# Kernel tuning notes

Hardware: AMD Instinct MI355X
Metric: run time of the kernel (lower is better)

## Reference

```python
import jax, jax.numpy as jnp
import numpy as np
import math

B, S = 4, 1024
V, D, L, H, F, MAXLEN = 32000, 1024, 6, 16, 4096, 2048
DH = D // H
NUM_BUCKETS, MAX_DIST = 32, 256
REL_SCALE = 64.0 ** 0.5
EPS = 1e-5


def setup_inputs() -> dict:
    key = jax.random.key(0)
    ks = iter(jax.random.split(key, 32))
    sd = 0.02
    inp = {
        'src': jax.random.randint(next(ks), (B, S), 0, V),
        'src_mask': jnp.ones((B, 1, 1, S), dtype=jnp.int32),
        'tok_emb': jax.random.normal(next(ks), (V, D), jnp.float32) * sd,
        'pos_emb': jax.random.normal(next(ks), (MAXLEN, D), jnp.float32) * sd,
        'Wq': jax.random.normal(next(ks), (L, D, D), jnp.float32) * sd,
        'bq': jnp.zeros((L, D), jnp.float32),
        'Wk': jax.random.normal(next(ks), (L, D, D), jnp.float32) * sd,
        'bk': jnp.zeros((L, D), jnp.float32),
        'Wv': jax.random.normal(next(ks), (L, D, D), jnp.float32) * sd,
        'bv': jnp.zeros((L, D), jnp.float32),
        'Wo': jax.random.normal(next(ks), (L, D, D), jnp.float32) * sd,
        'bo': jnp.zeros((L, D), jnp.float32),
        'rel_bias': jax.random.normal(next(ks), (L, NUM_BUCKETS, H), jnp.float32) * sd,
        'ln1_g': jnp.ones((L, D), jnp.float32),
        'ln1_b': jnp.zeros((L, D), jnp.float32),
        'W1': jax.random.normal(next(ks), (L, D, F), jnp.float32) * sd,
        'b1': jnp.zeros((L, F), jnp.float32),
        'W2': jax.random.normal(next(ks), (L, F, D), jnp.float32) * sd,
        'b2': jnp.zeros((L, D), jnp.float32),
        'ln2_g': jnp.ones((L, D), jnp.float32),
        'ln2_b': jnp.zeros((L, D), jnp.float32),
    }
    return inp


def _rel_pos_bucket(seq_len):
    # non-causal bucketing (T5-style), matching the torch source
    q = jnp.arange(seq_len)
    k = jnp.arange(seq_len)
    n = q[:, None] - k[None, :]          # == -(k - q)
    nb = NUM_BUCKETS // 2                # 16
    ret = (n < 0).astype(jnp.int32) * nb
    n = jnp.abs(n)
    max_exact = nb // 2                  # 8
    is_small = n < max_exact
    val_large = max_exact + (
        jnp.log(jnp.maximum(n, 1).astype(jnp.float32) / max_exact)
        / math.log(MAX_DIST / max_exact) * (nb - max_exact)
    ).astype(jnp.int32)
    val_large = jnp.minimum(val_large, nb - 1)
    return ret + jnp.where(is_small, n, val_large)  # [S,S] in [0,32)


def _layer_norm(x, g, b):
    mu = jnp.mean(x, axis=-1, keepdims=True)
    var = jnp.var(x, axis=-1, keepdims=True)
    return (x - mu) * jax.lax.rsqrt(var + EPS) * g + b


def reference(src, src_mask, tok_emb, pos_emb, Wq, bq, Wk, bk, Wv, bv, Wo, bo,
              rel_bias, ln1_g, ln1_b, W1, b1, W2, b2, ln2_g, ln2_b):
    seq_len = src.shape[1]
    bucket = _rel_pos_bucket(seq_len)                      # [S,S] int
    x = tok_emb[src] * jnp.sqrt(jnp.float32(D)) + pos_emb[jnp.arange(seq_len)][None]
    scale = jnp.sqrt(jnp.float32(DH))
    neg = jnp.float32(-1e10)

    def layer(x, p):
        (wq, bq_, wk, bk_, wv, bv_, wo, bo_, rb, g1, b1_, w1, bb1, w2, bb2, g2, b2_) = p
        Q = (x @ wq + bq_).reshape(B, seq_len, H, DH)
        K = (x @ wk + bk_).reshape(B, seq_len, H, DH)
        Vv = (x @ wv + bv_).reshape(B, seq_len, H, DH)
        energy = jnp.einsum('bqhd,bkhd->bhqk', Q, K) / scale
        energy = jnp.where(src_mask == 0, neg, energy)
        bias = rb[bucket]                                  # [S,S,H]
        energy = energy + jnp.transpose(bias, (2, 0, 1))[None] * REL_SCALE
        attn = jax.nn.softmax(energy, axis=-1)
        o = jnp.einsum('bhqk,bkhd->bqhd', attn, Vv).reshape(B, seq_len, D)
        o = o @ wo + bo_
        x = _layer_norm(x + o, g1, b1_)
        f = jax.nn.relu(x @ w1 + bb1) @ w2 + bb2
        x = _layer_norm(x + f, g2, b2_)
        return x, None

    params = (Wq, bq, Wk, bk, Wv, bv, Wo, bo, rel_bias,
              ln1_g, ln1_b, W1, b1, W2, b2, ln2_g, ln2_b)
    x, _ = jax.lax.scan(layer, x, params)
    return x
```

## Files before the change

### kernel.cpp

```cpp
#include <hip/hip_runtime.h>

#define B_ 4
#define S_ 1024
#define D_ 1024
#define F_ 4096
#define H_ 16
#define L_ 6
#define M_ (B_*S_)

#define LOG2E 1.44269504088896f

typedef unsigned short u16;
typedef __attribute__((ext_vector_type(4))) unsigned short u16x4;
typedef __attribute__((ext_vector_type(8))) short s16x8;
typedef __attribute__((ext_vector_type(8))) __bf16 bf16x8;
typedef __attribute__((ext_vector_type(4))) float f32x4;

typedef const __attribute__((address_space(1))) unsigned int gu32;
typedef __attribute__((address_space(3))) unsigned int su32;

__device__ __forceinline__ u16 f2bf(float f) {
  union { float f; unsigned u; } v; v.f = f;
  unsigned u = v.u;
  return (u16)((u + 0x7fffu + ((u >> 16) & 1u)) >> 16);
}
__device__ __forceinline__ float bf2f(u16 h) {
  union { unsigned u; float f; } v; v.u = (unsigned)h << 16; return v.f;
}

__device__ __forceinline__ f32x4 mfma16(s16x8 a, s16x8 b, f32x4 c) {
  return __builtin_amdgcn_mfma_f32_16x16x32_bf16(
      __builtin_bit_cast(bf16x8, a), __builtin_bit_cast(bf16x8, b), c, 0, 0, 0);
}

__device__ __forceinline__ void gload16(const void* g, void* s) {
  __builtin_amdgcn_global_load_lds((gu32*)g, (su32*)s, 16, 0, 0);
}

template<int OUTMODE>
__device__ __forceinline__ void gemm128_body(
    const u16* __restrict__ A, const u16* __restrict__ Bt,
    const float* __restrict__ b0, const float* __restrict__ b1,
    const float* __restrict__ b2, u16* __restrict__ Ch,
    u16* __restrict__ Vt, int N, int K, int kbeg, int kend)
{
  __shared__ __align__(16) u16 As[128 * 64];
  __shared__ __align__(16) u16 Bs[128 * 64];
  const int tid = threadIdx.x, lane = tid & 63, w = tid >> 6;
  const int bm = blockIdx.x * 128, bn = blockIdx.y * 128;
  const int wm = (w >> 1) * 64, wn = (w & 1) * 64;

  f32x4 acc[4][4];
#pragma unroll
  for (int i = 0; i < 4; i++)
#pragma unroll
    for (int j = 0; j < 4; j++) acc[i][j] = {0.f, 0.f, 0.f, 0.f};

  for (int k0 = kbeg; k0 < kend; k0 += 64) {
    __syncthreads();
#pragma unroll
    for (int i = 0; i < 4; i++) {
      const int flat = i * 4096 + w * 1024 + lane * 16;
      const int row = flat >> 7, ce = (flat & 127) >> 1;
      gload16(A + (size_t)(bm + row) * K + k0 + ce, As + i * 2048 + w * 512);
      gload16(Bt + (size_t)(bn + row) * K + k0 + ce, Bs + i * 2048 + w * 512);
    }
    __syncthreads();
#pragma unroll
    for (int kk = 0; kk < 2; kk++) {
      s16x8 af[4], bf[4];
#pragma unroll
      for (int mf = 0; mf < 4; mf++)
        af[mf] = *(const s16x8*)&As[(wm + mf * 16 + (lane & 15)) * 64 + kk * 32 + (lane >> 4) * 8];
#pragma unroll
      for (int nf = 0; nf < 4; nf++)
        bf[nf] = *(const s16x8*)&Bs[(wn + nf * 16 + (lane & 15)) * 64 + kk * 32 + (lane >> 4) * 8];
#pragma unroll
      for (int mf = 0; mf < 4; mf++)
#pragma unroll
        for (int nf = 0; nf < 4; nf++)
          acc[mf][nf] = mfma16(af[mf], bf[nf], acc[mf][nf]);
    }
  }

  if (OUTMODE == 3) {
    const int zz = bn >> 10;
    const int lcb = (bn & 1023) + wn;
    const float* bp = (zz == 0) ? b0 : (zz == 1) ? b1 : b2;
    if (zz == 2) {
      const int b = bm >> 10;
#pragma unroll
      for (int nf = 0; nf < 4; nf++) {
        const int dh2 = lcb + nf * 16 + (lane & 15);
        const int hq = dh2 >> 6, dh = dh2 & 63;
        const float bv = bp[dh2];
        u16* vrow = Vt + ((size_t)((b << 4) + hq) * 64 + dh) * S_;
#pragma unroll
        for (int mf = 0; mf < 4; mf++) {
          const int s0 = (bm & 1023) + wm + mf * 16 + ((lane >> 4) << 2);
          u16x4 hv;
#pragma unroll
          for (int j = 0; j < 4; j++) hv[j] = f2bf(acc[mf][nf][j] + bv);
          *(u16x4*)(vrow + s0) = hv;
        }
      }
    } else {
      const float sc = (zz == 0) ? (0.125f * LOG2E) : 1.0f;
      u16* Outz = Ch + (size_t)zz * M_ * D_;
#pragma unroll
      for (int nf = 0; nf < 4; nf++) {
        const int col = lcb + nf * 16 + (lane & 15);
        const float bv = bp[col];
#pragma unroll
        for (int mf = 0; mf < 4; mf++) {
#pragma unroll
          for (int j = 0; j < 4; j++) {
            const int row = bm + wm + mf * 16 + ((lane >> 4) << 2) + j;
            Outz[(size_t)row * D_ + col] = f2bf((acc[mf][nf][j] + bv) * sc);
          }
        }
      }
    }
  } else {
#pragma unroll
    for (int nf = 0; nf < 4; nf++) {
      const int col = bn + wn + nf * 16 + (lane & 15);
#pragma unroll
      for (int mf = 0; mf < 4; mf++) {
#pragma unroll
        for (int j = 0; j < 4; j++) {
          const int row = bm + wm + mf * 16 + ((lane >> 4) << 2) + j;
          Ch[(size_t)row * N + col] = f2bf(acc[mf][nf][j]);
        }
      }
    }
  }
}

__global__ __launch_bounds__(256, 3) void gemm_qkvf(
    const u16* __restrict__ A, const u16* __restrict__ WT,
    const float* __restrict__ bq, const float* __restrict__ bk,
    const float* __restrict__ bv, u16* __restrict__ Out, u16* __restrict__ Vt)
{
  gemm128_body<3>(A, WT, bq, bk, bv, Out, Vt, 3 * D_, D_, 0, D_);
}

__global__ __launch_bounds__(256, 3) void gemm_osplit2(
    const u16* __restrict__ A, const u16* __restrict__ WT,
    u16* __restrict__ P)
{
  const int z = blockIdx.z;
  gemm128_body<1>(A, WT, nullptr, nullptr, nullptr,
                  P + (size_t)z * M_ * D_, nullptr, D_, D_, z * 512, z * 512 + 512);
}

__device__ __forceinline__ s16x8 readfrag(const u16* half, int r, int kk, int hi4) {
  const int c = (kk * 64 + hi4 * 16) ^ ((r & 7) << 4);
  return *(const s16x8*)((const char*)half + r * 128 + c);
}

__device__ __forceinline__ void stage_half(
    const u16* __restrict__ src, int ldk, u16* lds_half, int w, int lane)
{
#pragma unroll
  for (int j = 0; j < 2; j++) {
    const int flat = j * 8192 + w * 1024 + lane * 16;
    const int row = flat >> 7;
    const int kb = (flat & 127) ^ ((row & 7) << 4);
    gload16(src + (size_t)row * ldk + (kb >> 1), lds_half + j * 4096 + w * 512);
  }
}

#define BAR     asm volatile("s_barrier" ::: "memory")
#define PH_PRE  asm volatile("s_barrier" ::: "memory"); __builtin_amdgcn_s_setprio(1)
#define PH_POST __builtin_amdgcn_s_setprio(0); __builtin_amdgcn_sched_barrier(0)
#define VM4     asm volatile("s_waitcnt vmcnt(4)" ::: "memory")
#define VM0     asm volatile("s_waitcnt vmcnt(0)" ::: "memory")

#define READ_B(bufhalf) do { \
  _Pragma("unroll") for (int nf = 0; nf < 4; nf++) \
  _Pragma("unroll") for (int kk = 0; kk < 2; kk++) \
    bfr[nf][kk] = readfrag(bufhalf, rb0 + nf * 16 + lo16, kk, hi4); } while (0)
#define READ_A(bufhalf, Q) do { \
  _Pragma("unroll") for (int m = 0; m < 2; m++) \
  _Pragma("unroll") for (int kk = 0; kk < 2; kk++) \
    af[m][kk] = readfrag(bufhalf, (2 * (Q) + m) * 16 + lo16, kk, hi4); } while (0)
#define DO_MFMA(Q) do { \
  _Pragma("unroll") for (int kk = 0; kk < 2; kk++) \
  _Pragma("unroll") for (int m = 0; m < 2; m++) \
  _Pragma("unroll") for (int nf = 0; nf < 4; nf++) \
    acc[2 * (Q) + m][nf] = mfma16(af[m][kk], bfr[nf][kk], acc[2 * (Q) + m][nf]); } while (0)

template<int OUTMODE>
__device__ __forceinline__ void gemm256_body(
    const u16* __restrict__ A, const u16* __restrict__ Bt,
    const float* __restrict__ bias, u16* __restrict__ Ch,
    int N, int K, int kbeg, int kslice)
{
  __shared__ __align__(16) u16 As[2][2][8192];
  __shared__ __align__(16) u16 Bs[2][2][8192];
  const int tid = threadIdx.x, lane = tid & 63, w = tid >> 6;
  const int wr = w >> 2, wc = w & 3;
  const int lo16 = lane & 15, hi4 = lane >> 4;
  const int bm = blockIdx.x * 256, bn = blockIdx.y * 256;
  const int rb0 = (wc & 1) * 64;

  const u16* Abase = A + (size_t)bm * K + kbeg;
  const u16* Bbase = Bt + (size_t)bn * K + kbeg;
  const size_t h1 = (size_t)128 * K;
  const int NT = kslice >> 6, NI = NT >> 1;

  f32x4 acc[8][4];
#pragma unroll
  for (int i = 0; i < 8; i++)
#pragma unroll
    for (int j = 0; j < 4; j++) acc[i][j] = {0.f, 0.f, 0.f, 0.f};

  stage_half(Abase,           K, As[0][0], w, lane);
  stage_half(Abase + h1,      K, As[0][1], w, lane);
  stage_half(Bbase,           K, Bs[0][0], w, lane);
  stage_half(Bbase + h1,      K, Bs[0][1], w, lane);
  stage_half(Abase + 64,      K, As[1][0], w, lane);
  stage_half(Abase + h1 + 64, K, As[1][1], w, lane);
  stage_half(Bbase + 64,      K, Bs[1][0], w, lane);
  stage_half(Bbase + h1 + 64, K, Bs[1][1], w, lane);
  asm volatile("s_waitcnt vmcnt(8)" ::: "memory");
  BAR;

  const u16* Ae = As[0][wr]; const u16* Ao = As[1][wr];
  const u16* Be = Bs[0][wc >> 1]; const u16* Bo = Bs[1][wc >> 1];
  s16x8 af[2][2], bfr[4][2];

  for (int it = 0; it < NI - 1; ++it) {
    READ_B(Be); READ_A(Ae, 0);
    if (it > 0) {
      stage_half(Abase +      (size_t)(2 * it + 1) * 64, K, As[1][0], w, lane);
      stage_half(Abase + h1 + (size_t)(2 * it + 1) * 64, K, As[1][1], w, lane);
    }
    PH_PRE; DO_MFMA(0); PH_POST; BAR;
    READ_A(Ae, 1);
    stage_half(Bbase +      (size_t)(2 * it + 2) * 64, K, Bs[0][0], w, lane);
    PH_PRE; DO_MFMA(1); PH_POST; BAR;
    READ_A(Ae, 2);
    stage_half(Bbase + h1 + (size_t)(2 * it + 2) * 64, K, Bs[0][1], w, lane);
    PH_PRE; DO_MFMA(2); PH_POST; BAR;
    READ_A(Ae, 3);
    PH_PRE; DO_MFMA(3); PH_POST; VM4; BAR;
    READ_B(Bo); READ_A(Ao, 0);
    stage_half(Abase +      (size_t)(2 * it + 2) * 64, K, As[0][0], w, lane);
    stage_half(Abase + h1 + (size_t)(2 * it + 2) * 64, K, As[0][1], w, lane);
    PH_PRE; DO_MFMA(0); PH_POST; BAR;
    READ_A(Ao, 1);
    stage_half(Bbase +      (size_t)(2 * it + 3) * 64, K, Bs[1][0], w, lane);
    PH_PRE; DO_MFMA(1); PH_POST; BAR;
    READ_A(Ao, 2);
    stage_half(Bbase + h1 + (size_t)(2 * it + 3) * 64, K, Bs[1][1], w, lane);
    PH_PRE; DO_MFMA(2); PH_POST; BAR;
    READ_A(Ao, 3);
    PH_PRE; DO_MFMA(3); PH_POST; VM4; BAR;
  }
  READ_B(Be); READ_A(Ae, 0);
  stage_half(Abase +      (size_t)(NT - 1) * 64, K, As[1][0], w, lane);
  stage_half(Abase + h1 + (size_t)(NT - 1) * 64, K, As[1][1], w, lane);
  PH_PRE; DO_MFMA(0); PH_POST; BAR;
  READ_A(Ae, 1);             PH_PRE; DO_MFMA(1); PH_POST; BAR;
  READ_A(Ae, 2);             PH_PRE; DO_MFMA(2); PH_POST; BAR;
  READ_A(Ae, 3);             PH_PRE; DO_MFMA(3); PH_POST; VM0; BAR;
  READ_B(Bo); READ_A(Ao, 0); PH_PRE; DO_MFMA(0); PH_POST; BAR;
  READ_A(Ao, 1);             PH_PRE; DO_MFMA(1); PH_POST; BAR;
  READ_A(Ao, 2);             PH_PRE; DO_MFMA(2); PH_POST; BAR;
  READ_A(Ao, 3);             PH_PRE; DO_MFMA(3); PH_POST;

  const int row0 = bm + wr * 128, col0 = bn + wc * 64;
#pragma unroll
  for (int nf = 0; nf < 4; nf++) {
    const int col = col0 + nf * 16 + lo16;
    const float bv = (OUTMODE == 2) ? bias[col] : 0.f;
#pragma unroll
    for (int mf = 0; mf < 8; mf++) {
#pragma unroll
      for (int j = 0; j < 4; j++) {
        const int row = row0 + mf * 16 + hi4 * 4 + j;
        float v = acc[mf][nf][j];
        if (OUTMODE == 2) v = fmaxf(v + bv, 0.f);
        Ch[(size_t)row * N + col] = f2bf(v);
      }
    }
  }
}

__global__ __launch_bounds__(512, 2) void gemm_ffn1(
    const u16* __restrict__ A, const u16* __restrict__ WT,
    const float* __restrict__ bias, u16* __restrict__ Out)
{
  gemm256_body<2>(A, WT, bias, Out, F_, D_, 0, D_);
}

__global__ __launch_bounds__(512, 2) void gemm_ffn2sp4(
    const u16* __restrict__ A, const u16* __restrict__ WT,
    u16* __restrict__ P)
{
  const int z = blockIdx.z;
  gemm256_body<4>(A, WT, nullptr, P + (size_t)z * M_ * D_,
                  D_, F_, z * 1024, 1024);
}

__global__ __launch_bounds__(256) void transpose_layer(
    const float* __restrict__ Wq, const float* __restrict__ Wk,
    const float* __restrict__ Wv, const float* __restrict__ Wo,
    const float* __restrict__ W1, const float* __restrict__ W2,
    u16* __restrict__ WT)
{
  __shared__ float tl[64][65];
  int bt = blockIdx.x;
  const float* src; u16* dst; int Rsrc, Csrc, cx, cy;
  if (bt < 1024) {
    const int m = bt >> 8; const int t = bt & 255;
    src = (m == 0) ? Wq : (m == 1) ? Wk : (m == 2) ? Wv : Wo;
    dst = WT + (size_t)m * 1024 * 1024;
    Rsrc = 1024; Csrc = 1024; cx = t & 15; cy = t >> 4;
  } else if (bt < 2048) {
    const int t = bt - 1024;
    src = W1; dst = WT + (size_t)4 * 1024 * 1024;
    Rsrc = 1024; Csrc = 4096; cx = t & 63; cy = t >> 6;
  } else {
    const int t = bt - 2048;
    src = W2; dst = WT + (size_t)8 * 1024 * 1024;
    Rsrc = 4096; Csrc = 1024; cx = t & 15; cy = t >> 4;
  }
  const int r0 = cy * 64, c0 = cx * 64;
  const int tid = threadIdx.x;
  const int rl = tid >> 2, q = tid & 3;
  const float* sp = src + (size_t)(r0 + rl) * Csrc + c0 + q * 16;
#pragma unroll
  for (int i = 0; i < 4; i++) {
    const float4 v = *(const float4*)(sp + i * 4);
    tl[rl][q * 16 + i * 4 + 0] = v.x;
    tl[rl][q * 16 + i * 4 + 1] = v.y;
    tl[rl][q * 16 + i * 4 + 2] = v.z;
    tl[rl][q * 16 + i * 4 + 3] = v.w;
  }
  __syncthreads();
#pragma unroll
  for (int it = 0; it < 2; it++) {
    const int idx = tid + it * 256;
    const int cl = idx >> 3, seg = idx & 7;
    const int rw0 = seg * 8;
    s16x8 v8;
#pragma unroll
    for (int u = 0; u < 8; u++) v8[u] = (short)f2bf(tl[rw0 + u][cl]);
    *(s16x8*)(dst + (size_t)(c0 + cl) * Rsrc + r0 + rw0) = v8;
  }
}

__global__ __launch_bounds__(256) void build_lut(
    const float* __restrict__ rb, float* __restrict__ lut_g)
{
  const int h = blockIdx.x, l = blockIdx.y;
  for (int idx = threadIdx.x; idx < 2048; idx += 256) {
    const int rel = idx - 1024;
    const int ret = rel < 0 ? 16 : 0;
    const int n = rel < 0 ? -rel : rel;
    int bu;
    if (n < 8) bu = ret + n;
    else {
      const float t = logf((float)n * 0.125f) * (8.0f / 3.4657359027997265f);
      int vl = 8 + (int)t;
      if (vl > 15) vl = 15;
      bu = ret + vl;
    }
    lut_g[(size_t)(l * H_ + h) * 2048 + idx] = rb[l * 512 + bu * 16 + h] * (8.0f * LOG2E);
  }
}

__global__ __launch_bounds__(256) void mask2neg(
    const int* __restrict__ mask, u16* __restrict__ mf)
{
  const int i = blockIdx.x * 256 + threadIdx.x;
  if (i < B_ * S_) mf[i] = mask[i] ? (u16)0 : f2bf(-1e10f * LOG2E);
}

__device__ __forceinline__ s16x8 lds_swz(const u16* base, int row, int cb) {
  const int addr = row * 128 + (cb ^ ((row & 7) << 4));
  return *(const s16x8*)((const char*)base + addr);
}

#define ATTN_STAGE(t, buf) do { \
  const int kt2 = (t) * 64; \
  const int flat2 = tid * 16; \
  const int row2 = flat2 >> 7; \
  const int ce2 = ((flat2 & 127) ^ ((row2 & 7) << 4)) >> 1; \
  gload16(Kb + (size_t)(bS + kt2 + row2) * D_ + hh + ce2, Ks[buf] + w * 512); \
  gload16(Vt + (size_t)(bh * 64 + row2) * S_ + kt2 + ce2, Vs[buf] + w * 512); \
} while (0)

__global__ __launch_bounds__(512, 2) void attn_kernel(
    const u16* __restrict__ Qb, const u16* __restrict__ Kb,
    const u16* __restrict__ Vt, const u16* __restrict__ mask16,
    const float* __restrict__ lut_g, u16* __restrict__ AO)
{
  __shared__ __align__(16) float lut[2048];
  __shared__ __align__(16) u16 maskf[1024];
  __shared__ __align__(16) u16 Ks[2][64 * 64];
  __shared__ __align__(16) u16 Vs[2][64 * 64];
  __shared__ __align__(16) u16 Ps[8][16 * 68];

  const int tid = threadIdx.x;
  const int lane = tid & 63;
  const int w = tid >> 6;
  const int bh = blockIdx.x;
  const int b = bh >> 4, h = bh & 15;
  const int q0 = blockIdx.y * 128 + w * 16;
  const int bS = b * S_, hh = h * 64;
  const int lo16 = lane & 15, hi4 = lane >> 4;

  const float* lsrc = lut_g + (size_t)h * 2048;
  gload16(lsrc + w * 256 + lane * 4, lut + w * 256);
  if (w < 2)
    gload16(mask16 + bS + w * 512 + lane * 8, maskf + w * 512);

  s16x8 qf[2];
#pragma unroll
  for (int kk = 0; kk < 2; kk++)
    qf[kk] = *(const s16x8*)(Qb + (size_t)(bS + q0 + lo16) * D_ + hh +
                             kk * 32 + hi4 * 8);

  s16x8 onesf;
#pragma unroll
  for (int u = 0; u < 8; u++) onesf[u] = (short)((lo16 == 0) ? 0x3F80 : 0);

  f32x4 oacc[5];
#pragma unroll
  for (int i = 0; i < 5; i++) oacc[i] = {0.f, 0.f, 0.f, 0.f};

  ATTN_STAGE(0, 0);
  asm volatile("s_waitcnt vmcnt(0) lgkmcnt(0)" ::: "memory");
  __builtin_amdgcn_s_barrier();

  for (int t = 0; t < S_ / 64; ++t) {
    const int cur = t & 1;
    const int kt = t * 64;
    if (t < S_ / 64 - 1) ATTN_STAGE(t + 1, cur ^ 1);

    f32x4 sacc[4];
#pragma unroll
    for (int i = 0; i < 4; i++) sacc[i] = {0.f, 0.f, 0.f, 0.f};
#pragma unroll
    for (int kk = 0; kk < 2; kk++) {
      const int cb = kk * 64 + hi4 * 16;
#pragma unroll
      for (int nf = 0; nf < 4; nf++) {
        const s16x8 kb = lds_swz(Ks[cur], nf * 16 + lo16, cb);
        sacc[nf] = mfma16(qf[kk], kb, sacc[nf]);
      }
    }

    float kmf[4];
#pragma unroll
    for (int nf = 0; nf < 4; nf++)
      kmf[nf] = bf2f(maskf[kt + nf * 16 + lo16]);

    const int lidx0 = q0 + hi4 * 4 + 1024 - kt - lo16;
#pragma unroll
    for (int j = 0; j < 4; j++) {
      const int lrow = (hi4 << 2) + j;
#pragma unroll
      for (int nf = 0; nf < 4; nf++) {
        const float s = sacc[nf][j] + kmf[nf] + lut[lidx0 + j - nf * 16];
        Ps[w][lrow * 68 + nf * 16 + lo16] = f2bf(__builtin_amdgcn_exp2f(s));
      }
    }

#pragma unroll
    for (int kk = 0; kk < 2; kk++) {
      const s16x8 pa = *(const s16x8*)&Ps[w][lo16 * 68 + kk * 32 + hi4 * 8];
      const int cb = kk * 64 + hi4 * 16;
#pragma unroll
      for (int df = 0; df < 4; df++) {
        const s16x8 vb = lds_swz(Vs[cur], df * 16 + lo16, cb);
        oacc[df] = mfma16(pa, vb, oacc[df]);
      }
      oacc[4] = mfma16(pa, onesf, oacc[4]);
    }

    asm volatile("s_waitcnt vmcnt(0)" ::: "memory");
    __builtin_amdgcn_s_barrier();
  }

  float inv[4];
#pragma unroll
  for (int j = 0; j < 4; j++) {
    const float l = __shfl(oacc[4][j], lane & 48);
    inv[j] = 1.0f / l;
  }
#pragma unroll
  for (int df = 0; df < 4; df++)
#pragma unroll
    for (int j = 0; j < 4; j++) {
      const int qrow = q0 + (hi4 << 2) + j;
      AO[(size_t)(bS + qrow) * D_ + hh + df * 16 + lo16] =
          f2bf(oacc[df][j] * inv[j]);
    }
}

template<int NP>
__global__ __launch_bounds__(256) void ln_fusedb(
    const u16* __restrict__ Xh, const u16* __restrict__ P,
    const float* __restrict__ bias, const float* __restrict__ g,
    const float* __restrict__ be, u16* __restrict__ Yh, float* __restrict__ Yf)
{
  const int row = blockIdx.x;
  const int tid = threadIdx.x;
  const size_t off = (size_t)row * D_;
  const size_t ps = (size_t)M_ * D_;
  const u16x4 xv = ((const u16x4*)(Xh + off))[tid];
  float v[4];
#pragma unroll
  for (int q = 0; q < 4; q++) v[q] = bf2f(xv[q]);
#pragma unroll
  for (int p = 0; p < NP; p++) {
    const u16x4 pv = ((const u16x4*)(P + p * ps + off))[tid];
#pragma unroll
    for (int q = 0; q < 4; q++) v[q] += bf2f(pv[q]);
  }
  const float4 bb = ((const float4*)bias)[tid];
  v[0] += bb.x; v[1] += bb.y; v[2] += bb.z; v[3] += bb.w;

  float sum = v[0] + v[1] + v[2] + v[3];
  float ss = v[0] * v[0] + v[1] * v[1] + v[2] * v[2] + v[3] * v[3];
#pragma unroll
  for (int o = 1; o < 64; o <<= 1) {
    sum += __shfl_xor(sum, o);
    ss += __shfl_xor(ss, o);
  }
  __shared__ float s1[4], s2[4];
  if ((tid & 63) == 0) { s1[tid >> 6] = sum; s2[tid >> 6] = ss; }
  __syncthreads();
  sum = s1[0] + s1[1] + s1[2] + s1[3];
  ss = s2[0] + s2[1] + s2[2] + s2[3];
  const float mu = sum * (1.f / D_);
  const float var = ss * (1.f / D_) - mu * mu;
  const float rstd = rsqrtf(var + 1e-5f);
  const float4 gv = ((const float4*)g)[tid];
  const float4 bv = ((const float4*)be)[tid];
  float y[4];
  y[0] = (v[0] - mu) * rstd * gv.x + bv.x;
  y[1] = (v[1] - mu) * rstd * gv.y + bv.y;
  y[2] = (v[2] - mu) * rstd * gv.z + bv.z;
  y[3] = (v[3] - mu) * rstd * gv.w + bv.w;
  u16x4 hv;
  hv.x = f2bf(y[0]); hv.y = f2bf(y[1]); hv.z = f2bf(y[2]); hv.w = f2bf(y[3]);
  ((u16x4*)(Yh + off))[tid] = hv;
  if (Yf != nullptr) {
    float4 yf; yf.x = y[0]; yf.y = y[1]; yf.z = y[2]; yf.w = y[3];
    ((float4*)(Yf + off))[tid] = yf;
  }
}

__global__ __launch_bounds__(256) void embed_kernel(
    const int* __restrict__ src, const float* __restrict__ tok,
    const float* __restrict__ pos, u16* __restrict__ Xh)
{
  const int row = blockIdx.x;
  const int s = row & (S_ - 1);
  const int t = src[row];
  const int tid = threadIdx.x;
  const float4 tv = ((const float4*)(tok + (size_t)t * D_))[tid];
  const float4 pv = ((const float4*)(pos + (size_t)s * D_))[tid];
  u16x4 hv;
  hv.x = f2bf(tv.x * 32.f + pv.x);
  hv.y = f2bf(tv.y * 32.f + pv.y);
  hv.z = f2bf(tv.z * 32.f + pv.z);
  hv.w = f2bf(tv.w * 32.f + pv.w);
  ((u16x4*)(Xh + (size_t)row * D_))[tid] = hv;
}

extern "C" void kernel_launch(void* const* d_in, const int* in_sizes, int n_in,
                              void* d_out, int out_size, void* d_ws, size_t ws_size,
                              hipStream_t stream)
{
  const int* src = (const int*)d_in[0];
  const int* mask = (const int*)d_in[1];
  const float* tok_emb = (const float*)d_in[2];
  const float* pos_emb = (const float*)d_in[3];
  const float* Wq = (const float*)d_in[4];
  const float* bq = (const float*)d_in[5];
  const float* Wk = (const float*)d_in[6];
  const float* bk = (const float*)d_in[7];
  const float* Wv = (const float*)d_in[8];
  const float* bv = (const float*)d_in[9];
  const float* Wo = (const float*)d_in[10];
  const float* bo = (const float*)d_in[11];
  const float* rb = (const float*)d_in[12];
  const float* g1 = (const float*)d_in[13];
  const float* b1n = (const float*)d_in[14];
  const float* W1 = (const float*)d_in[15];
  const float* b1f = (const float*)d_in[16];
  const float* W2 = (const float*)d_in[17];
  const float* b2f = (const float*)d_in[18];
  const float* g2 = (const float*)d_in[19];
  const float* b2n = (const float*)d_in[20];
  float* out = (float*)d_out;

  char* ws = (char*)d_ws;
  const size_t MB = 1ull << 20;
  u16* xb16  = (u16*)(ws + 0);
  u16* Qb16  = (u16*)(ws + 8 * MB);
  u16* Kb16  = (u16*)(ws + 16 * MB);
  u16* Vt16  = (u16*)(ws + 24 * MB);
  u16* AO16  = (u16*)(ws + 32 * MB);
  u16* Pp16  = (u16*)(ws + 40 * MB);
  u16* WT    = (u16*)(ws + 72 * MB);
  u16* Hb16  = (u16*)(ws + 8 * MB);
  float* lut_g  = (float*)(ws + 96 * MB);
  u16*   mask16 = (u16*)(ws + 96 * MB + 786432);

  u16* WTqkv = WT;
  u16* WTo   = WT + (size_t)3 * 1024 * 1024;
  u16* WT1   = WT + (size_t)4 * 1024 * 1024;
  u16* WT2   = WT + (size_t)8 * 1024 * 1024;

  embed_kernel<<<M_, 256, 0, stream>>>(src, tok_emb, pos_emb, xb16);
  build_lut<<<dim3(H_, L_), 256, 0, stream>>>(rb, lut_g);
  mask2neg<<<(B_ * S_ + 255) / 256, 256, 0, stream>>>(mask, mask16);

  for (int l = 0; l < L_; l++) {
    const size_t oDD = (size_t)l * D_ * D_;
    const size_t oDF = (size_t)l * D_ * F_;

    transpose_layer<<<3072, 256, 0, stream>>>(
        Wq + oDD, Wk + oDD, Wv + oDD, Wo + oDD, W1 + oDF, W2 + oDF, WT);

    gemm_qkvf<<<dim3(M_ / 128, 3 * D_ / 128), 256, 0, stream>>>(
        xb16, WTqkv, bq + l * D_, bk + l * D_, bv + l * D_, Qb16, Vt16);

    attn_kernel<<<dim3(B_ * H_, S_ / 128), 512, 0, stream>>>(
        Qb16, Kb16, Vt16, mask16, lut_g + (size_t)l * H_ * 2048, AO16);

    gemm_osplit2<<<dim3(M_ / 128, D_ / 128, 2), 256, 0, stream>>>(
        AO16, WTo, Pp16);

    ln_fusedb<2><<<M_, 256, 0, stream>>>(
        xb16, Pp16, bo + l * D_, g1 + l * D_, b1n + l * D_, xb16, nullptr);

    gemm_ffn1<<<dim3(M_ / 256, F_ / 256), 512, 0, stream>>>(
        xb16, WT1, b1f + l * F_, Hb16);

    gemm_ffn2sp4<<<dim3(M_ / 256, D_ / 256, 4), 512, 0, stream>>>(
        Hb16, WT2, Pp16);

    ln_fusedb<4><<<M_, 256, 0, stream>>>(
        xb16, Pp16, b2f + l * D_, g2 + l * D_, b2n + l * D_, xb16,
        (l == L_ - 1) ? out : nullptr);
  }
}
```

Baseline: 1.239 ms.

## Triple-buffer K/V tiles in attention with one barrier per tile and MFMA priority

Moves the attention kernel's K/V staging from double to triple buffering. Loads are issued two tiles ahead, and each iteration waits with a partial vmcnt, so global loads overlap more compute and only one barrier is needed per tile. It also wraps the MFMA sections in s_setprio so matrix ops get issue priority over other waves. The cost is extra LDS (two more 8KB buffers), which could affect the two-blocks-per-CU occupancy, and the lgkmcnt wait on the initial LUT/mask loads is removed.

After: 1.233 ms (median of 2 runs). Within noise of the previous version (-0.5%).

```diff
diff --git a/kernel.cpp b/kernel.cpp
--- a/kernel.cpp
+++ b/kernel.cpp
@@ -394,6 +394,42 @@
   gload16(Vt + (size_t)(bh * 64 + row2) * S_ + kt2 + ce2, Vs[buf] + w * 512); \
 } while (0)
 
+#define ATTN_TILE(bc, kt) do { \
+    f32x4 sacc[4]; \
+    _Pragma("unroll") for (int i = 0; i < 4; i++) sacc[i] = {0.f, 0.f, 0.f, 0.f}; \
+    __builtin_amdgcn_s_setprio(1); \
+    _Pragma("unroll") for (int kk = 0; kk < 2; kk++) { \
+      const int cb = kk * 64 + hi4 * 16; \
+      _Pragma("unroll") for (int nf = 0; nf < 4; nf++) { \
+        const s16x8 kb = lds_swz(Ks[bc], nf * 16 + lo16, cb); \
+        sacc[nf] = mfma16(qf[kk], kb, sacc[nf]); \
+      } \
+    } \
+    __builtin_amdgcn_s_setprio(0); \
+    float kmf[4]; \
+    _Pragma("unroll") for (int nf = 0; nf < 4; nf++) \
+      kmf[nf] = bf2f(maskf[(kt) + nf * 16 + lo16]); \
+    const int lidx0 = q0 + hi4 * 4 + 1024 - (kt) - lo16; \
+    _Pragma("unroll") for (int j = 0; j < 4; j++) { \
+      const int lrow = (hi4 << 2) + j; \
+      _Pragma("unroll") for (int nf = 0; nf < 4; nf++) { \
+        const float s = sacc[nf][j] + kmf[nf] + lut[lidx0 + j - nf * 16]; \
+        Ps[w][lrow * 68 + nf * 16 + lo16] = f2bf(__builtin_amdgcn_exp2f(s)); \
+      } \
+    } \
+    __builtin_amdgcn_s_setprio(1); \
+    _Pragma("unroll") for (int kk = 0; kk < 2; kk++) { \
+      const s16x8 pa = *(const s16x8*)&Ps[w][lo16 * 68 + kk * 32 + hi4 * 8]; \
+      const int cb = kk * 64 + hi4 * 16; \
+      _Pragma("unroll") for (int df = 0; df < 4; df++) { \
+        const s16x8 vb = lds_swz(Vs[bc], df * 16 + lo16, cb); \
+        oacc[df] = mfma16(pa, vb, oacc[df]); \
+      } \
+      oacc[4] = mfma16(pa, onesf, oacc[4]); \
+    } \
+    __builtin_amdgcn_s_setprio(0); \
+} while (0)
+
 __global__ __launch_bounds__(512, 2) void attn_kernel(
     const u16* __restrict__ Qb, const u16* __restrict__ Kb,
     const u16* __restrict__ Vt, const u16* __restrict__ mask16,
@@ -401,8 +437,8 @@
 {
   __shared__ __align__(16) float lut[2048];
   __shared__ __align__(16) u16 maskf[1024];
-  __shared__ __align__(16) u16 Ks[2][64 * 64];
-  __shared__ __align__(16) u16 Vs[2][64 * 64];
+  __shared__ __align__(16) u16 Ks[3][64 * 64];
+  __shared__ __align__(16) u16 Vs[3][64 * 64];
   __shared__ __align__(16) u16 Ps[8][16 * 68];
 
   const int tid = threadIdx.x;
@@ -434,57 +470,21 @@
   for (int i = 0; i < 5; i++) oacc[i] = {0.f, 0.f, 0.f, 0.f};
 
   ATTN_STAGE(0, 0);
-  asm volatile("s_waitcnt vmcnt(0) lgkmcnt(0)" ::: "memory");
-  __builtin_amdgcn_s_barrier();
-
-  for (int t = 0; t < S_ / 64; ++t) {
-    const int cur = t & 1;
+  ATTN_STAGE(1, 1);
+
+  for (int t = 0; t < S_ / 64 - 1; ++t) {
+    const int bc = t % 3;
     const int kt = t * 64;
-    if (t < S_ / 64 - 1) ATTN_STAGE(t + 1, cur ^ 1);
-
-    f32x4 sacc[4];
-#pragma unroll
-    for (int i = 0; i < 4; i++) sacc[i] = {0.f, 0.f, 0.f, 0.f};
-#pragma unroll
-    for (int kk = 0; kk < 2; kk++) {
-      const int cb = kk * 64 + hi4 * 16;
-#pragma unroll
-      for (int nf = 0; nf < 4; nf++) {
-        const s16x8 kb = lds_swz(Ks[cur], nf * 16 + lo16, cb);
-        sacc[nf] = mfma16(qf[kk], kb, sacc[nf]);
-      }
-    }
-
-    float kmf[4];
-#pragma unroll
-    for (int nf = 0; nf < 4; nf++)
-      kmf[nf] = bf2f(maskf[kt + nf * 16 + lo16]);
-
-    const int lidx0 = q0 + hi4 * 4 + 1024 - kt - lo16;
-#pragma unroll
-    for (int j = 0; j < 4; j++) {
-      const int lrow = (hi4 << 2) + j;
-#pragma unroll
-      for (int nf = 0; nf < 4; nf++) {
-        const float s = sacc[nf][j] + kmf[nf] + lut[lidx0 + j - nf * 16];
-        Ps[w][lrow * 68 + nf * 16 + lo16] = f2bf(__builtin_amdgcn_exp2f(s));
-      }
-    }
-
-#pragma unroll
-    for (int kk = 0; kk < 2; kk++) {
-      const s16x8 pa = *(const s16x8*)&Ps[w][lo16 * 68 + kk * 32 + hi4 * 8];
-      const int cb = kk * 64 + hi4 * 16;
-#pragma unroll
-      for (int df = 0; df < 4; df++) {
-        const s16x8 vb = lds_swz(Vs[cur], df * 16 + lo16, cb);
-        oacc[df] = mfma16(pa, vb, oacc[df]);
-      }
-      oacc[4] = mfma16(pa, onesf, oacc[4]);
-    }
-
+    asm volatile("s_waitcnt vmcnt(2)" ::: "memory");
+    __builtin_amdgcn_s_barrier();
+    if (t + 2 < S_ / 64) ATTN_STAGE(t + 2, (t + 2) % 3);
+    ATTN_TILE(bc, kt);
+  }
+  {
+    const int t = S_ / 64 - 1;
     asm volatile("s_waitcnt vmcnt(0)" ::: "memory");
     __builtin_amdgcn_s_barrier();
+    ATTN_TILE(t % 3, t * 64);
   }
 
   float inv[4];
```
